# Kernel tuning notes

Hardware: AMD Instinct MI355X
Metric: run time of the kernel (lower is better)

The kernel has to match this reference:

```python
import jax, jax.numpy as jnp
import numpy as np


def setup_inputs() -> dict:
    key = jax.random.key(0)
    ks = jax.random.split(key, 8)
    T, S, W, O = 50000, 168, 336, 48
    N = T - W - O + 1
    x = jax.random.uniform(ks[0], (T,), minval=0.5, maxval=1.5, dtype=jnp.float32)
    noise = jax.random.normal(ks[1], (N, W), dtype=jnp.float32) * 0.001  # Normal(0, std=0.001)
    level_sc = jax.random.uniform(ks[2], (), minval=-1.0, maxval=1.0, dtype=jnp.float32)
    seas_sc = jax.random.uniform(ks[3], (), minval=-1.0, maxval=1.0, dtype=jnp.float32)
    init_seas = jax.random.uniform(ks[4], (S,), minval=0.65, maxval=1.35, dtype=jnp.float32)
    W1 = jax.random.normal(ks[5], (W, W), dtype=jnp.float32) / np.float32(np.sqrt(W))
    b1 = jnp.zeros((W,), jnp.float32)
    W2 = jax.random.normal(ks[6], (W, O), dtype=jnp.float32) / np.float32(np.sqrt(W))
    b2 = jnp.zeros((O,), jnp.float32)
    return {"x": x, "noise": noise, "level_sc": level_sc, "seas_sc": seas_sc,
            "init_seas": init_seas, "W1": W1, "b1": b1, "W2": W2, "b2": b2,
            "window_size": W, "out_size": O, "lvp": 1}


def reference(x, noise, level_sc, seas_sc, init_seas, W1, b1, W2, b2,
              window_size, out_size, lvp):
    T = x.shape[0]
    a = jax.nn.sigmoid(level_sc)      # level smoothing coeff
    g = jax.nn.sigmoid(seas_sc)       # seasonal smoothing coeff
    s0 = jnp.exp(init_seas)           # [S] initial multiplicative seasonals
    # seasonals list in torch: seas[0..S-1]=s0, seas[S]=s0[0], seas[S+i]=w_i.
    # Ring buffer holds seas[i..i+S-1] at step i (starting i=1): [s0[1:], s0[0]].
    buf0 = jnp.concatenate([s0[1:], s0[:1]])
    level0 = x[0] / s0[0]

    def step(carry, xi):
        level, buf = carry
        seas_i = buf[0]
        new_level = a * xi / seas_i + (1.0 - a) * level
        new_w = g * xi / new_level + (1.0 - g) * seas_i
        new_buf = jnp.concatenate([buf[1:], new_w[None]])
        return (new_level, new_buf), (new_level, new_w, jnp.log(new_level / level))

    _, (lvls, ws, logdiffs) = jax.lax.scan(step, (level0, buf0), x[1:])
    levels = jnp.concatenate([level0[None], lvls])        # [T]
    seas_full = jnp.concatenate([s0, s0[:1], ws])         # [S+T]

    d = logdiffs[1:] - logdiffs[:-1]
    level_var_loss = jnp.mean(d * d) * lvp

    N = T - window_size - out_size + 1
    idx_in = jnp.arange(N)[:, None] + jnp.arange(window_size)[None, :]   # [N,W]
    idx_lab = jnp.arange(N)[:, None] + window_size + jnp.arange(out_size)[None, :]  # [N,O]
    lev = levels[jnp.arange(N) + window_size][:, None]    # [N,1]
    inp = jnp.log(x[idx_in] / (lev * seas_full[idx_in])) + noise   # noisy squashed inputs
    labels = jnp.log(x[idx_lab] / (lev * seas_full[idx_lab]))

    h = jnp.tanh(inp @ W1 + b1)        # tanh_no_lstm: Linear(336,336)+tanh
    out = h @ W2 + b2                  # linear_no_lstm: Linear(336,48)
    return out, labels, level_var_loss
```

## Files before the change

kernel.cpp:

```cpp
#include <hip/hip_runtime.h>
#include <hip/hip_bf16.h>

typedef __attribute__((ext_vector_type(8))) short  s16x8;
typedef __attribute__((ext_vector_type(4))) short  s16x4;
typedef __attribute__((ext_vector_type(4))) float  f32x4;

#define T_LEN 50000
#define S_LEN 168
#define W_IN  336
#define O_OUT 48
#define N_ROWS (T_LEN - W_IN - O_OUT + 1)
#define N_PAD  49664
#define NBLK   (N_PAD / 64)

__device__ inline short f2bf(float f) {
    union { float f; unsigned u; } v; v.f = f;
    unsigned u = v.u;
    unsigned r = u + 0x7fffu + ((u >> 16) & 1u);
    return (short)(r >> 16);
}

__device__ inline int bfpk(float lo, float hi) {
    float2 f2; f2.x = lo; f2.y = hi;
    __hip_bfloat162 h = __float22bfloat162_rn(f2);
    int r; __builtin_memcpy(&r, &h, 4);
    return r;
}

__device__ inline float readlane_f(float v, int l) {
    return __int_as_float(__builtin_amdgcn_readlane(__float_as_int(v), l));
}

__device__ inline float fast_tanh(float v) {
    float e = __expf(2.f * v);
    return 1.f - 2.f * __builtin_amdgcn_rcpf(e + 1.f);
}

__global__ void k_preconvert(const float* __restrict__ W1, const float* __restrict__ W2,
                             short* __restrict__ W1T, short* __restrict__ W2T) {
    int idx = blockIdx.x * 256 + threadIdx.x;
    const int n1 = 352 * 352;
    const int n2 = n1 + 48 * 360;
    if (idx < n1) {
        int j = idx / 352, k = idx % 352;
        W1T[idx] = (j < 336 && k < 336) ? f2bf(W1[k * 336 + j]) : (short)0;
    } else if (idx < n2) {
        int i2 = idx - n1;
        int o = i2 / 360, k = i2 % 360;
        W2T[i2] = (k < 336) ? f2bf(W2[k * 48 + o]) : (short)0;
    }
}

#define DPP_FMA(q_, CTRL, W, RM) { \
    int t_ = __builtin_amdgcn_update_dpp(0, __float_as_int(q_), (CTRL), (RM), 0xf, true); \
    q_ = fmaf((W), __int_as_float(t_), q_); }

__global__ void k_scan(const float* __restrict__ x, const float* __restrict__ level_sc,
                       const float* __restrict__ seas_sc, const float* __restrict__ init_seas,
                       float* __restrict__ lw, float* __restrict__ seasinit) {
    int lane = threadIdx.x;
    float a = 1.f / (1.f + expf(-level_sc[0]));
    float g = 1.f / (1.f + expf(-seas_sc[0]));
    float om = 1.f - a, omg = 1.f - g;

    for (int t = lane; t <= S_LEN; t += 64)
        seasinit[t] = expf(init_seas[t < S_LEN ? t : 0]);

    float lpv = x[0] / expf(init_seas[0]);
    if (lane == 0) { lw[0] = lpv; lw[1] = 1.f; }

    float om1 = om, om2v = om1 * om1, om4 = om2v * om2v, om8 = om4 * om4;
    float pl    = powf(om, (float)(lane + 1));
    float fpre  = powf(om, (float)((lane & 15) + 1));
    float fpre2 = powf(om, (float)((lane & 31) + 1));

    int  idx4 = ((lane + 24) & 63) << 2;
    bool lowj = (lane < 40);

#define SCAN(QOUT, XV, RSV) { \
    float q_ = a * (XV) * (RSV); \
    DPP_FMA(q_, 0x111, om1,  0xf); \
    DPP_FMA(q_, 0x112, om2v, 0xf); \
    DPP_FMA(q_, 0x114, om4,  0xf); \
    DPP_FMA(q_, 0x118, om8,  0xf); \
    DPP_FMA(q_, 0x142, fpre,  0xa); \
    DPP_FMA(q_, 0x143, fpre2, 0xc); \
    QOUT = q_; }

#define XLOAD(I) float xr##I = x[1 + 64 * I + lane];
    XLOAD(0) XLOAD(1) XLOAD(2) XLOAD(3) XLOAD(4) XLOAD(5) XLOAD(6) XLOAD(7)
    XLOAD(8) XLOAD(9) XLOAD(10) XLOAD(11) XLOAD(12) XLOAD(13) XLOAD(14) XLOAD(15)
#undef XLOAD

    float sW = expf(init_seas[1 + lane]);
    float sN = expf(init_seas[65 + lane]);
    int t105 = 105 + lane;
    float wPrev = expf(init_seas[t105 >= S_LEN ? 0 : t105]);
    float Qcur; SCAN(Qcur, xr0, __builtin_amdgcn_rcpf(sW));
    int ib = 1;

#define BODY(R, RN, CLAMP) { \
    float lvl = fmaf(pl, lpv, Qcur); \
    lpv = readlane_f(lvl, 63); \
    float w_ = fmaf(omg, sW, (g * xr##R) * __builtin_amdgcn_rcpf(lvl)); \
    float2 pk_; pk_.x = lvl; pk_.y = w_; \
    *(float2*)&lw[2 * (ib + lane)] = pk_; \
    int tA_ = __builtin_amdgcn_ds_bpermute(idx4, __float_as_int(wPrev)); \
    int tB_ = __builtin_amdgcn_ds_bpermute(idx4, __float_as_int(w_)); \
    float sNN_ = lowj ? __int_as_float(tA_) : __int_as_float(tB_); \
    float Qn_; SCAN(Qn_, xr##RN, __builtin_amdgcn_rcpf(sN)); \
    int pidx = ib + 1024 + lane; \
    if (CLAMP) pidx = pidx > (T_LEN - 1) ? (T_LEN - 1) : pidx; \
    xr##R = x[pidx]; \
    Qcur = Qn_; sW = sN; sN = sNN_; wPrev = w_; \
    ib += 64; }

    for (int kb = 0; kb < 47; ++kb) {
        BODY(0,1,0)  BODY(1,2,0)  BODY(2,3,0)  BODY(3,4,0)
        BODY(4,5,0)  BODY(5,6,0)  BODY(6,7,0)  BODY(7,8,0)
        BODY(8,9,0)  BODY(9,10,0) BODY(10,11,0) BODY(11,12,0)
        BODY(12,13,0) BODY(13,14,0) BODY(14,15,0) BODY(15,0,0)
    }
    BODY(0,1,0)  BODY(1,2,0)  BODY(2,3,0)  BODY(3,4,0)
    BODY(4,5,0)  BODY(5,6,0)  BODY(6,7,0)  BODY(7,8,0)
    BODY(8,9,0)  BODY(9,10,0) BODY(10,11,0) BODY(11,12,0)
    BODY(12,13,0)
    BODY(13,14,1) BODY(14,15,1) BODY(15,0,1)
    BODY(0,1,1)  BODY(1,2,1)  BODY(2,3,1)  BODY(3,4,1)
    BODY(4,5,1)  BODY(5,6,1)  BODY(6,7,1)  BODY(7,8,1)
    BODY(8,9,1)  BODY(9,10,1) BODY(10,11,1) BODY(11,12,1)
#undef BODY

    {
        float lvl = fmaf(pl, lpv, Qcur);
        lpv = readlane_f(lvl, 63);
        float w_ = fmaf(omg, sW, (g * xr12) * __builtin_amdgcn_rcpf(lvl));
        float2 pk_; pk_.x = lvl; pk_.y = w_;
        *(float2*)&lw[2 * (49921 + lane)] = pk_;
    }
    {
        float Qn_; SCAN(Qn_, xr13, __builtin_amdgcn_rcpf(sN));
        float lvl = fmaf(pl, lpv, Qn_);
        if (lane < 15) {
            float w_ = fmaf(omg, sN, (g * xr13) * __builtin_amdgcn_rcpf(lvl));
            float2 pk_; pk_.x = lvl; pk_.y = w_;
            *(float2*)&lw[2 * (49985 + lane)] = pk_;
        }
    }
#undef SCAN
}

__global__ void k_logs(const float* __restrict__ x, const float* __restrict__ lw,
                       const float* __restrict__ seasinit,
                       float* __restrict__ F, float* __restrict__ llev,
                       float* __restrict__ partials) {
    __shared__ float sm[258];
    __shared__ float red[256];
    int tid = threadIdx.x;
    int t = blockIdx.x * 256 + tid;
    float ll = 0.f;
    if (t < T_LEN) {
        float2 cur = *(const float2*)&lw[2 * t];
        int ps = t - S_LEN; if (ps < 0) ps = 0;
        float sv = (t <= S_LEN) ? seasinit[t] : lw[2 * ps + 1];
        F[t]  = __logf(x[t]) - __logf(sv);
        ll    = __logf(cur.x);
        llev[t] = ll;
    }
    sm[tid] = ll;
    if (tid < 2) {
        int te = blockIdx.x * 256 + 256 + tid;
        sm[256 + tid] = (te < T_LEN) ? __logf(lw[2 * te]) : 0.f;
    }
    __syncthreads();
    float s = 0.f;
    if (t < T_LEN - 2) {
        float d = sm[tid + 2] - 2.f * sm[tid + 1] + sm[tid];
        s = d * d;
    }
    red[tid] = s; __syncthreads();
    for (int off = 128; off > 0; off >>= 1) {
        if (tid < off) red[tid] += red[tid + off];
        __syncthreads();
    }
    if (tid == 0) partials[blockIdx.x] = red[0];
}

__global__ __launch_bounds__(256) void k_prep(
        const float* __restrict__ noise, const float* __restrict__ F,
        const float* __restrict__ llev, short* __restrict__ inpbf,
        float* __restrict__ labels) {
    __shared__ float Flds[448];
    __shared__ float Llds[64];
    int t = threadIdx.x;
    long n0 = (long)blockIdx.x * 64;
    if (t < 112)      *(f32x4*)&Flds[t * 4] = *(const f32x4*)&F[n0 + t * 4];
    else if (t < 128) *(f32x4*)&Llds[(t - 112) * 4] = *(const f32x4*)&llev[n0 + W_IN + (t - 112) * 4];
    __syncthreads();

#pragma unroll
    for (int i = 0; i < 11; ++i) {
        int c = t + 256 * i;
        int r = c / 44, kc = c - r * 44;
        int k0 = kc * 8;
        long n = n0 + r;
        int4 s = {0, 0, 0, 0};
        if (n < N_ROWS && k0 < W_IN) {
            float lv = Llds[r];
            const float* np = &noise[n * (long)W_IN + k0];
            f32x4 nz0 = *(const f32x4*)&np[0];
            f32x4 nz1 = *(const f32x4*)&np[4];
            const float* fp = &Flds[r + k0];
            s.x = bfpk(fp[0] - lv + nz0[0], fp[1] - lv + nz0[1]);
            s.y = bfpk(fp[2] - lv + nz0[2], fp[3] - lv + nz0[3]);
            s.z = bfpk(fp[4] - lv + nz1[0], fp[5] - lv + nz1[1]);
            s.w = bfpk(fp[6] - lv + nz1[2], fp[7] - lv + nz1[3]);
        }
        *(int4*)&inpbf[n * 352 + k0] = s;
    }
#pragma unroll
    for (int i = 0; i < 3; ++i) {
        int c = t + 256 * i;
        int r = c / 12, cc = (c - r * 12) * 4;
        long n = n0 + r;
        if (n < N_ROWS) {
            float lv = Llds[r];
            const float* fp = &Flds[r + W_IN + cc];
            f32x4 v;
            v[0] = fp[0] - lv; v[1] = fp[1] - lv; v[2] = fp[2] - lv; v[3] = fp[3] - lv;
            *(f32x4*)&labels[n * O_OUT + cc] = v;
        }
    }
}

__global__ __launch_bounds__(256, 3) void k_gemm(
        const short* __restrict__ inpbf, const short* __restrict__ W1T,
        const float* __restrict__ b1, const short* __restrict__ W2T,
        const float* __restrict__ b2, const float* __restrict__ partials,
        const int* __restrict__ lvp, float* __restrict__ out,
        float* __restrict__ loss) {
    __shared__ __align__(16) short hlds[64][360];
    __shared__ __align__(16) float b1lds[352];

    int t = threadIdx.x, w = t >> 6, l = t & 63;
    int lm = l & 15, lq = l >> 4;
    long n0 = (long)blockIdx.x * 64;

    if (blockIdx.x == 0 && w == 3) {
        float s = partials[l] + partials[l + 64] + partials[l + 128];
        if (l < 4) s += partials[l + 192];
#pragma unroll
        for (int off = 32; off > 0; off >>= 1) s += __shfl_down(s, off, 64);
        if (l == 0) loss[0] = s / (float)(T_LEN - 2) * (float)lvp[0];
    }

    if (t < 88) {
        int i4 = t * 4;
        f32x4 v = (f32x4){0.f, 0.f, 0.f, 0.f};
        if (i4 < W_IN) v = *(const f32x4*)&b1[i4];
        *(f32x4*)&b1lds[i4] = v;
    }

    int rbase = (w >> 1) * 32;
    int jbase = (w & 1) * 176;
    const short* arow0 = inpbf + (n0 + rbase + lm) * 352 + lq * 8;
    const short* arow1 = arow0 + 16 * 352;

    f32x4 acc0[11], acc1[11];
#pragma unroll
    for (int c = 0; c < 11; ++c) { acc0[c] = (f32x4){0,0,0,0}; acc1[c] = (f32x4){0,0,0,0}; }

    const short* w1row = &W1T[(jbase + lm) * 352 + lq * 8];
#define LDW(CT, KS) (*(const s16x8*)&w1row[(CT) * 5632 + (KS) * 32])
    s16x8 af0 = LDW(0,0), af1 = LDW(1,0), af2 = LDW(2,0),
          af3 = LDW(3,0), af4 = LDW(4,0), af5 = LDW(5,0);
    s16x8 bA0 = *(const s16x8*)&arow0[0];
    s16x8 bA1 = *(const s16x8*)&arow1[0];

#define MM2(CT, AF) \
    acc0[CT] = __builtin_amdgcn_mfma_f32_16x16x32_bf16(AF, b0, acc0[CT], 0, 0, 0); \
    acc1[CT] = __builtin_amdgcn_mfma_f32_16x16x32_bf16(AF, bb1, acc1[CT], 0, 0, 0);

#define KSTEP_R(KS, A0,A1,A2,A3,A4,A5) { \
    s16x8 b0 = bA0, bb1 = bA1; \
    if ((KS) < 10) { \
        bA0 = *(const s16x8*)&arow0[((KS)+1) * 32]; \
        bA1 = *(const s16x8*)&arow1[((KS)+1) * 32]; \
    } \
    MM2(0, A0)   A0 = LDW(6, (KS)); \
    MM2(1, A1)   A1 = LDW(7, (KS)); \
    MM2(2, A2)   A2 = LDW(8, (KS)); \
    MM2(3, A3)   A3 = LDW(9, (KS)); \
    MM2(4, A4)   A4 = LDW(10, (KS)); \
    MM2(5, A5)   if ((KS) < 10) A5 = LDW(0, (KS)+1); \
    MM2(6, A0)   if ((KS) < 10) A0 = LDW(1, (KS)+1); \
    MM2(7, A1)   if ((KS) < 10) A1 = LDW(2, (KS)+1); \
    MM2(8, A2)   if ((KS) < 10) A2 = LDW(3, (KS)+1); \
    MM2(9, A3)   if ((KS) < 10) A3 = LDW(4, (KS)+1); \
    MM2(10, A4)  if ((KS) < 10) A4 = LDW(5, (KS)+1); \
}

    KSTEP_R(0,  af0,af1,af2,af3,af4,af5)
    KSTEP_R(1,  af5,af0,af1,af2,af3,af4)
    KSTEP_R(2,  af4,af5,af0,af1,af2,af3)
    KSTEP_R(3,  af3,af4,af5,af0,af1,af2)
    KSTEP_R(4,  af2,af3,af4,af5,af0,af1)
    KSTEP_R(5,  af1,af2,af3,af4,af5,af0)
    KSTEP_R(6,  af0,af1,af2,af3,af4,af5)
    KSTEP_R(7,  af5,af0,af1,af2,af3,af4)
    KSTEP_R(8,  af4,af5,af0,af1,af2,af3)
    KSTEP_R(9,  af3,af4,af5,af0,af1,af2)
    KSTEP_R(10, af2,af3,af4,af5,af0,af1)
#undef KSTEP_R
#undef MM2
#undef LDW

    __syncthreads();

#pragma unroll
    for (int ct = 0; ct < 11; ++ct) {
        f32x4 b1q = *(f32x4*)&b1lds[jbase + ct * 16 + lq * 4];
        int2 p0, p1;
        p0.x = bfpk(fast_tanh(acc0[ct][0] + b1q[0]), fast_tanh(acc0[ct][1] + b1q[1]));
        p0.y = bfpk(fast_tanh(acc0[ct][2] + b1q[2]), fast_tanh(acc0[ct][3] + b1q[3]));
        p1.x = bfpk(fast_tanh(acc1[ct][0] + b1q[0]), fast_tanh(acc1[ct][1] + b1q[1]));
        p1.y = bfpk(fast_tanh(acc1[ct][2] + b1q[2]), fast_tanh(acc1[ct][3] + b1q[3]));
        *(int2*)&hlds[rbase + lm][jbase + ct * 16 + lq * 4]      = p0;
        *(int2*)&hlds[rbase + 16 + lm][jbase + ct * 16 + lq * 4] = p1;
    }
    __syncthreads();

    f32x4 a2[3];
    a2[0] = (f32x4){0,0,0,0}; a2[1] = (f32x4){0,0,0,0}; a2[2] = (f32x4){0,0,0,0};
#pragma unroll
    for (int ks = 0; ks < 11; ++ks) {
        s16x8 hf = *(s16x8*)&hlds[w * 16 + lm][ks * 32 + lq * 8];
#pragma unroll
        for (int ct = 0; ct < 3; ++ct) {
            s16x8 bf2 = *(const s16x8*)&W2T[(ct * 16 + lm) * 360 + ks * 32 + lq * 8];
            a2[ct] = __builtin_amdgcn_mfma_f32_16x16x32_bf16(hf, bf2, a2[ct], 0, 0, 0);
        }
    }
    int rloc = w * 16 + lq * 4;
#pragma unroll
    for (int ct = 0; ct < 3; ++ct) {
        float b2v = b2[ct * 16 + lm];
#pragma unroll
        for (int r = 0; r < 4; ++r) {
            long row = n0 + rloc + r;
            if (row < N_ROWS) out[row * O_OUT + ct * 16 + lm] = a2[ct][r] + b2v;
        }
    }
}

extern "C" void kernel_launch(void* const* d_in, const int* in_sizes, int n_in,
                              void* d_out, int out_size, void* d_ws, size_t ws_size,
                              hipStream_t stream) {
    const float* x         = (const float*)d_in[0];
    const float* noise     = (const float*)d_in[1];
    const float* level_sc  = (const float*)d_in[2];
    const float* seas_sc   = (const float*)d_in[3];
    const float* init_seas = (const float*)d_in[4];
    const float* W1        = (const float*)d_in[5];
    const float* b1        = (const float*)d_in[6];
    const float* W2        = (const float*)d_in[7];
    const float* b2        = (const float*)d_in[8];
    const int*   lvp       = (const int*)d_in[11];

    float* out    = (float*)d_out;
    float* labels = out + (long)N_ROWS * O_OUT;
    float* loss   = labels + (long)N_ROWS * O_OUT;

    float* wsf      = (float*)d_ws;
    float* lw       = wsf;
    float* seasinit = wsf + 100096;
    float* F        = wsf + 100288;
    float* llev     = wsf + 150464;
    float* partials = wsf + 200512;
    short* W1T      = (short*)(wsf + 200768);
    short* W2T      = W1T + 352 * 352;
    short* inpbf    = (short*)(wsf + 271360);

    k_preconvert<<<552, 256, 0, stream>>>(W1, W2, W1T, W2T);
    k_scan<<<1, 64, 0, stream>>>(x, level_sc, seas_sc, init_seas, lw, seasinit);
    k_logs<<<196, 256, 0, stream>>>(x, lw, seasinit, F, llev, partials);
    k_prep<<<NBLK, 256, 0, stream>>>(noise, F, llev, inpbf, labels);
    k_gemm<<<NBLK, 256, 0, stream>>>(inpbf, W1T, b1, W2T, b2, partials, lvp, out, loss);
}
```

Baseline: 148.9 us.

## Fuse weight preconversion into scan kernel and use 56-lane chunks without bpermute

The weight bf16 transpose/convert kernel is folded into the serial scan launch as extra blocks, so one launch is removed and the conversion runs alongside the single-wave scan. The scan now advances 56 timesteps per chunk instead of 64. With 168 = 3·56, the seasonal value needed three chunks later is exactly the lane's own earlier w, which removes the two ds_bpermute cross-lane shuffles and the select from the serial dependency chain. The trade-off is more chunk iterations (about 893 instead of 782) and idle lanes 56-63, plus a per-step store bound check.

```diff
diff --git a/kernel.cpp b/kernel.cpp
--- a/kernel.cpp
+++ b/kernel.cpp
@@ -36,28 +36,31 @@
     return 1.f - 2.f * __builtin_amdgcn_rcpf(e + 1.f);
 }
 
-__global__ void k_preconvert(const float* __restrict__ W1, const float* __restrict__ W2,
-                             short* __restrict__ W1T, short* __restrict__ W2T) {
-    int idx = blockIdx.x * 256 + threadIdx.x;
-    const int n1 = 352 * 352;
-    const int n2 = n1 + 48 * 360;
-    if (idx < n1) {
-        int j = idx / 352, k = idx % 352;
-        W1T[idx] = (j < 336 && k < 336) ? f2bf(W1[k * 336 + j]) : (short)0;
-    } else if (idx < n2) {
-        int i2 = idx - n1;
-        int o = i2 / 360, k = i2 % 360;
-        W2T[i2] = (k < 336) ? f2bf(W2[k * 48 + o]) : (short)0;
-    }
-}
-
 #define DPP_FMA(q_, CTRL, W, RM) { \
     int t_ = __builtin_amdgcn_update_dpp(0, __float_as_int(q_), (CTRL), (RM), 0xf, true); \
     q_ = fmaf((W), __int_as_float(t_), q_); }
 
-__global__ void k_scan(const float* __restrict__ x, const float* __restrict__ level_sc,
-                       const float* __restrict__ seas_sc, const float* __restrict__ init_seas,
-                       float* __restrict__ lw, float* __restrict__ seasinit) {
+__global__ __launch_bounds__(256) void k_scanpre(
+        const float* __restrict__ x, const float* __restrict__ level_sc,
+        const float* __restrict__ seas_sc, const float* __restrict__ init_seas,
+        float* __restrict__ lw, float* __restrict__ seasinit,
+        const float* __restrict__ W1, const float* __restrict__ W2,
+        short* __restrict__ W1T, short* __restrict__ W2T) {
+    if (blockIdx.x != 0) {
+        int idx = (blockIdx.x - 1) * 256 + threadIdx.x;
+        const int n1 = 352 * 352;
+        const int n2 = n1 + 48 * 360;
+        if (idx < n1) {
+            int j = idx / 352, k = idx % 352;
+            W1T[idx] = (j < 336 && k < 336) ? f2bf(W1[k * 336 + j]) : (short)0;
+        } else if (idx < n2) {
+            int i2 = idx - n1;
+            int o = i2 / 360, k = i2 % 360;
+            W2T[i2] = (k < 336) ? f2bf(W2[k * 48 + o]) : (short)0;
+        }
+        return;
+    }
+    if (threadIdx.x >= 64) return;
     int lane = threadIdx.x;
     float a = 1.f / (1.f + expf(-level_sc[0]));
     float g = 1.f / (1.f + expf(-seas_sc[0]));
@@ -73,9 +76,6 @@
     float pl    = powf(om, (float)(lane + 1));
     float fpre  = powf(om, (float)((lane & 15) + 1));
     float fpre2 = powf(om, (float)((lane & 31) + 1));
-
-    int  idx4 = ((lane + 24) & 63) << 2;
-    bool lowj = (lane < 40);
 
 #define SCAN(QOUT, XV, RSV) { \
     float q_ = a * (XV) * (RSV); \
@@ -87,66 +87,46 @@
     DPP_FMA(q_, 0x143, fpre2, 0xc); \
     QOUT = q_; }
 
-#define XLOAD(I) float xr##I = x[1 + 64 * I + lane];
+#define XLOAD(I) float xr##I = x[1 + 56 * I + lane];
     XLOAD(0) XLOAD(1) XLOAD(2) XLOAD(3) XLOAD(4) XLOAD(5) XLOAD(6) XLOAD(7)
     XLOAD(8) XLOAD(9) XLOAD(10) XLOAD(11) XLOAD(12) XLOAD(13) XLOAD(14) XLOAD(15)
 #undef XLOAD
 
-    float sW = expf(init_seas[1 + lane]);
-    float sN = expf(init_seas[65 + lane]);
-    int t105 = 105 + lane;
-    float wPrev = expf(init_seas[t105 >= S_LEN ? 0 : t105]);
-    float Qcur; SCAN(Qcur, xr0, __builtin_amdgcn_rcpf(sW));
+    float sc = expf(init_seas[1 + lane]);
+    float sn = expf(init_seas[57 + lane]);
+    int i2x = 113 + lane;
+    float wprev = expf(init_seas[i2x >= S_LEN ? i2x - S_LEN : i2x]);
+
+    float Qc; SCAN(Qc, xr0, __builtin_amdgcn_rcpf(sc));
+    float Qn; SCAN(Qn, xr1, __builtin_amdgcn_rcpf(sn));
     int ib = 1;
 
-#define BODY(R, RN, CLAMP) { \
-    float lvl = fmaf(pl, lpv, Qcur); \
-    lpv = readlane_f(lvl, 63); \
-    float w_ = fmaf(omg, sW, (g * xr##R) * __builtin_amdgcn_rcpf(lvl)); \
-    float2 pk_; pk_.x = lvl; pk_.y = w_; \
-    *(float2*)&lw[2 * (ib + lane)] = pk_; \
-    int tA_ = __builtin_amdgcn_ds_bpermute(idx4, __float_as_int(wPrev)); \
-    int tB_ = __builtin_amdgcn_ds_bpermute(idx4, __float_as_int(w_)); \
-    float sNN_ = lowj ? __int_as_float(tA_) : __int_as_float(tB_); \
-    float Qn_; SCAN(Qn_, xr##RN, __builtin_amdgcn_rcpf(sN)); \
-    int pidx = ib + 1024 + lane; \
-    if (CLAMP) pidx = pidx > (T_LEN - 1) ? (T_LEN - 1) : pidx; \
+#define BODY(R, R2) { \
+    float lvl = fmaf(pl, lpv, Qc); \
+    lpv = readlane_f(lvl, 55); \
+    float w_ = fmaf(omg, sc, (g * xr##R) * __builtin_amdgcn_rcpf(lvl)); \
+    int lim = T_LEN - ib; \
+    if (lane < (lim < 56 ? lim : 56)) { \
+        float2 pk_; pk_.x = lvl; pk_.y = w_; \
+        *(float2*)&lw[2 * (ib + lane)] = pk_; \
+    } \
+    float Qnew; SCAN(Qnew, xr##R2, __builtin_amdgcn_rcpf(wprev)); \
+    int pidx = ib + 896 + lane; pidx = pidx > (T_LEN - 1) ? (T_LEN - 1) : pidx; \
     xr##R = x[pidx]; \
-    Qcur = Qn_; sW = sN; sN = sNN_; wPrev = w_; \
-    ib += 64; }
-
-    for (int kb = 0; kb < 47; ++kb) {
-        BODY(0,1,0)  BODY(1,2,0)  BODY(2,3,0)  BODY(3,4,0)
-        BODY(4,5,0)  BODY(5,6,0)  BODY(6,7,0)  BODY(7,8,0)
-        BODY(8,9,0)  BODY(9,10,0) BODY(10,11,0) BODY(11,12,0)
-        BODY(12,13,0) BODY(13,14,0) BODY(14,15,0) BODY(15,0,0)
-    }
-    BODY(0,1,0)  BODY(1,2,0)  BODY(2,3,0)  BODY(3,4,0)
-    BODY(4,5,0)  BODY(5,6,0)  BODY(6,7,0)  BODY(7,8,0)
-    BODY(8,9,0)  BODY(9,10,0) BODY(10,11,0) BODY(11,12,0)
-    BODY(12,13,0)
-    BODY(13,14,1) BODY(14,15,1) BODY(15,0,1)
-    BODY(0,1,1)  BODY(1,2,1)  BODY(2,3,1)  BODY(3,4,1)
-    BODY(4,5,1)  BODY(5,6,1)  BODY(6,7,1)  BODY(7,8,1)
-    BODY(8,9,1)  BODY(9,10,1) BODY(10,11,1) BODY(11,12,1)
+    Qc = Qn; Qn = Qnew; sc = sn; sn = wprev; wprev = w_; \
+    ib += 56; }
+
+    for (int kb = 0; kb < 55; ++kb) {
+        BODY(0,2)   BODY(1,3)   BODY(2,4)   BODY(3,5)
+        BODY(4,6)   BODY(5,7)   BODY(6,8)   BODY(7,9)
+        BODY(8,10)  BODY(9,11)  BODY(10,12) BODY(11,13)
+        BODY(12,14) BODY(13,15) BODY(14,0)  BODY(15,1)
+    }
+    BODY(0,2)   BODY(1,3)   BODY(2,4)   BODY(3,5)
+    BODY(4,6)   BODY(5,7)   BODY(6,8)   BODY(7,9)
+    BODY(8,10)  BODY(9,11)  BODY(10,12) BODY(11,13)
+    BODY(12,14)
 #undef BODY
-
-    {
-        float lvl = fmaf(pl, lpv, Qcur);
-        lpv = readlane_f(lvl, 63);
-        float w_ = fmaf(omg, sW, (g * xr12) * __builtin_amdgcn_rcpf(lvl));
-        float2 pk_; pk_.x = lvl; pk_.y = w_;
-        *(float2*)&lw[2 * (49921 + lane)] = pk_;
-    }
-    {
-        float Qn_; SCAN(Qn_, xr13, __builtin_amdgcn_rcpf(sN));
-        float lvl = fmaf(pl, lpv, Qn_);
-        if (lane < 15) {
-            float w_ = fmaf(omg, sN, (g * xr13) * __builtin_amdgcn_rcpf(lvl));
-            float2 pk_; pk_.x = lvl; pk_.y = w_;
-            *(float2*)&lw[2 * (49985 + lane)] = pk_;
-        }
-    }
 #undef SCAN
 }
 
@@ -381,8 +361,8 @@
     short* W2T      = W1T + 352 * 352;
     short* inpbf    = (short*)(wsf + 271360);
 
-    k_preconvert<<<552, 256, 0, stream>>>(W1, W2, W1T, W2T);
-    k_scan<<<1, 64, 0, stream>>>(x, level_sc, seas_sc, init_seas, lw, seasinit);
+    k_scanpre<<<553, 256, 0, stream>>>(x, level_sc, seas_sc, init_seas, lw, seasinit,
+                                       W1, W2, W1T, W2T);
     k_logs<<<196, 256, 0, stream>>>(x, lw, seasinit, F, llev, partials);
     k_prep<<<NBLK, 256, 0, stream>>>(noise, F, llev, inpbf, labels);
     k_gemm<<<NBLK, 256, 0, stream>>>(inpbf, W1T, b1, W2T, b2, partials, lvp, out, loss);
```

Result: slower. 159.5 us (+7.1%).

## Fuse input preparation into GEMM kernel via shared-memory staging

Applied to the files above, without the earlier changes.

Merges the k_prep kernel into k_gemm: each block now builds its 64x352 bf16 input tile directly in LDS, in a buffer shared with the hidden-activation tile, and writes the labels at the end. This removes the global round trip of the bf16 input matrix (about 35 MB written and read back) and one kernel launch. The trade-offs are that the GEMM A-operand now comes from LDS with possible bank conflicts, the fused kernel holds more LDS per block which may lower occupancy, and the noise loads are no longer overlapped by a separate kernel.

```diff
diff --git a/kernel.cpp b/kernel.cpp
--- a/kernel.cpp
+++ b/kernel.cpp
@@ -186,16 +186,40 @@
     if (tid == 0) partials[blockIdx.x] = red[0];
 }
 
-__global__ __launch_bounds__(256) void k_prep(
+__global__ __launch_bounds__(256, 3) void k_gemm(
         const float* __restrict__ noise, const float* __restrict__ F,
-        const float* __restrict__ llev, short* __restrict__ inpbf,
-        float* __restrict__ labels) {
-    __shared__ float Flds[448];
-    __shared__ float Llds[64];
-    int t = threadIdx.x;
+        const float* __restrict__ llev, const short* __restrict__ W1T,
+        const float* __restrict__ b1, const short* __restrict__ W2T,
+        const float* __restrict__ b2, const float* __restrict__ partials,
+        const int* __restrict__ lvp, float* __restrict__ out,
+        float* __restrict__ labels, float* __restrict__ loss) {
+    __shared__ __align__(16) char  uni[46080];
+    __shared__ __align__(16) float Flds[448];
+    __shared__ __align__(16) float Llds[64];
+    __shared__ __align__(16) float b1lds[352];
+    short (*inp)[352]  = (short(*)[352])uni;
+    short (*hlds)[360] = (short(*)[360])uni;
+
+    int t = threadIdx.x, w = t >> 6, l = t & 63;
+    int lm = l & 15, lq = l >> 4;
     long n0 = (long)blockIdx.x * 64;
+
+    if (blockIdx.x == 0 && w == 3) {
+        float s = partials[l] + partials[l + 64] + partials[l + 128];
+        if (l < 4) s += partials[l + 192];
+#pragma unroll
+        for (int off = 32; off > 0; off >>= 1) s += __shfl_down(s, off, 64);
+        if (l == 0) loss[0] = s / (float)(T_LEN - 2) * (float)lvp[0];
+    }
+
     if (t < 112)      *(f32x4*)&Flds[t * 4] = *(const f32x4*)&F[n0 + t * 4];
     else if (t < 128) *(f32x4*)&Llds[(t - 112) * 4] = *(const f32x4*)&llev[n0 + W_IN + (t - 112) * 4];
+    else if (t < 216) {
+        int i4 = (t - 128) * 4;
+        f32x4 v = (f32x4){0.f, 0.f, 0.f, 0.f};
+        if (i4 < W_IN) v = *(const f32x4*)&b1[i4];
+        *(f32x4*)&b1lds[i4] = v;
+    }
     __syncthreads();
 
 #pragma unroll
@@ -216,55 +240,14 @@
             s.z = bfpk(fp[4] - lv + nz1[0], fp[5] - lv + nz1[1]);
             s.w = bfpk(fp[6] - lv + nz1[2], fp[7] - lv + nz1[3]);
         }
-        *(int4*)&inpbf[n * 352 + k0] = s;
-    }
-#pragma unroll
-    for (int i = 0; i < 3; ++i) {
-        int c = t + 256 * i;
-        int r = c / 12, cc = (c - r * 12) * 4;
-        long n = n0 + r;
-        if (n < N_ROWS) {
-            float lv = Llds[r];
-            const float* fp = &Flds[r + W_IN + cc];
-            f32x4 v;
-            v[0] = fp[0] - lv; v[1] = fp[1] - lv; v[2] = fp[2] - lv; v[3] = fp[3] - lv;
-            *(f32x4*)&labels[n * O_OUT + cc] = v;
-        }
-    }
-}
-
-__global__ __launch_bounds__(256, 3) void k_gemm(
-        const short* __restrict__ inpbf, const short* __restrict__ W1T,
-        const float* __restrict__ b1, const short* __restrict__ W2T,
-        const float* __restrict__ b2, const float* __restrict__ partials,
-        const int* __restrict__ lvp, float* __restrict__ out,
-        float* __restrict__ loss) {
-    __shared__ __align__(16) short hlds[64][360];
-    __shared__ __align__(16) float b1lds[352];
-
-    int t = threadIdx.x, w = t >> 6, l = t & 63;
-    int lm = l & 15, lq = l >> 4;
-    long n0 = (long)blockIdx.x * 64;
-
-    if (blockIdx.x == 0 && w == 3) {
-        float s = partials[l] + partials[l + 64] + partials[l + 128];
-        if (l < 4) s += partials[l + 192];
-#pragma unroll
-        for (int off = 32; off > 0; off >>= 1) s += __shfl_down(s, off, 64);
-        if (l == 0) loss[0] = s / (float)(T_LEN - 2) * (float)lvp[0];
-    }
-
-    if (t < 88) {
-        int i4 = t * 4;
-        f32x4 v = (f32x4){0.f, 0.f, 0.f, 0.f};
-        if (i4 < W_IN) v = *(const f32x4*)&b1[i4];
-        *(f32x4*)&b1lds[i4] = v;
-    }
+        *(int4*)&inp[r][k0] = s;
+    }
+    __syncthreads();
 
     int rbase = (w >> 1) * 32;
     int jbase = (w & 1) * 176;
-    const short* arow0 = inpbf + (n0 + rbase + lm) * 352 + lq * 8;
-    const short* arow1 = arow0 + 16 * 352;
+    const short* arow0 = &inp[rbase + lm][lq * 8];
+    const short* arow1 = &inp[rbase + 16 + lm][lq * 8];
 
     f32x4 acc0[11], acc1[11];
 #pragma unroll
@@ -351,6 +334,20 @@
             if (row < N_ROWS) out[row * O_OUT + ct * 16 + lm] = a2[ct][r] + b2v;
         }
     }
+
+#pragma unroll
+    for (int i = 0; i < 3; ++i) {
+        int c = t + 256 * i;
+        int r = c / 12, cc = (c - r * 12) * 4;
+        long n = n0 + r;
+        if (n < N_ROWS) {
+            float lv = Llds[r];
+            const float* fp = &Flds[r + W_IN + cc];
+            f32x4 v;
+            v[0] = fp[0] - lv; v[1] = fp[1] - lv; v[2] = fp[2] - lv; v[3] = fp[3] - lv;
+            *(f32x4*)&labels[n * O_OUT + cc] = v;
+        }
+    }
 }
 
 extern "C" void kernel_launch(void* const* d_in, const int* in_sizes, int n_in,
@@ -379,11 +376,10 @@
     float* partials = wsf + 200512;
     short* W1T      = (short*)(wsf + 200768);
     short* W2T      = W1T + 352 * 352;
-    short* inpbf    = (short*)(wsf + 271360);
 
     k_preconvert<<<552, 256, 0, stream>>>(W1, W2, W1T, W2T);
     k_scan<<<1, 64, 0, stream>>>(x, level_sc, seas_sc, init_seas, lw, seasinit);
     k_logs<<<196, 256, 0, stream>>>(x, lw, seasinit, F, llev, partials);
-    k_prep<<<NBLK, 256, 0, stream>>>(noise, F, llev, inpbf, labels);
-    k_gemm<<<NBLK, 256, 0, stream>>>(inpbf, W1T, b1, W2T, b2, partials, lvp, out, loss);
-}
+    k_gemm<<<NBLK, 256, 0, stream>>>(noise, F, llev, W1T, b1, W2T, b2,
+                                     partials, lvp, out, labels, loss);
+}
```

Measured after the change: 144.3 us. -3.1%, faster.
